# Performance work log

Hardware: AMD Instinct MI355X
Metric: run time of the kernel (lower is better)

Reference implementation:

```python
import jax, jax.numpy as jnp
import numpy as np

B, N, E = 64, 2048, 32768          # graphs, nodes/graph, edges/graph
DIM = 64
RATIO = 0.8
K1 = int(np.ceil(RATIO * N))        # 1639 nodes/graph after pool1
K2 = int(np.ceil(RATIO * K1))       # 1312 nodes/graph after pool2
NUM_CLASSES = 6


def gcn_conv(x, W, b, src, dst, valid, n):
    # GCNConv with self-loops: out = D^-1/2 (A+I) D^-1/2 (x W) + b
    xw = x @ W                                          # [n, DIM]
    deg = jnp.zeros(n, x.dtype).at[dst].add(valid) + 1.0  # in-degree incl. self-loop
    norm = valid * jax.lax.rsqrt(deg[src] * deg[dst])      # per-edge norm (0 for masked)
    agg = jnp.zeros_like(xw).at[dst].add(xw[src] * norm[:, None])
    return agg + xw / deg[:, None] + b                  # self-loop term has norm 1/deg


def topk_pool(x, p, n_graphs, n_per, k):
    # PyG TopKPooling: score = tanh(x.p/||p||); keep top-k per graph; gate x by score
    score = jnp.tanh((x @ p) / jnp.linalg.norm(p))       # [n_graphs*n_per]
    vals, idx = jax.lax.top_k(score.reshape(n_graphs, n_per), k)  # [n_graphs, k]
    xg = x.reshape(n_graphs, n_per, -1)
    sel = jnp.take_along_axis(xg, idx[..., None], axis=1)          # [n_graphs, k, DIM]
    xp = sel * vals[..., None]
    perm = (idx + (jnp.arange(n_graphs) * n_per)[:, None]).reshape(-1)  # global ids kept
    return xp.reshape(n_graphs * k, -1), perm


def global_max_mean(x, n_graphs, n_per):
    xg = x.reshape(n_graphs, n_per, -1)
    return jnp.concatenate([xg.max(axis=1), xg.mean(axis=1)], axis=1)  # [n_graphs, 2*DIM]


def forward(x, edge_index, batch, W1, b1, p1, W2, b2, p2, lin1_w, lin1_b, lin2_w, lin2_b):
    src, dst = edge_index[0], edge_index[1]
    n_total = B * N
    ones = jnp.ones(src.shape[0], x.dtype)

    x = jax.nn.relu(gcn_conv(x, W1, b1, src, dst, ones, n_total))
    x, perm = topk_pool(x, p1, B, N, K1)
    x1 = global_max_mean(x, B, K1)

    # filter_adj: reindex edges to surviving nodes; drop (mask) edges touching removed nodes
    new_id = jnp.full(n_total, -1, jnp.int32).at[perm].set(jnp.arange(B * K1, dtype=jnp.int32))
    s2, d2 = new_id[src], new_id[dst]
    valid = ((s2 >= 0) & (d2 >= 0)).astype(x.dtype)
    s2 = jnp.where(s2 >= 0, s2, 0)
    d2 = jnp.where(d2 >= 0, d2, 0)

    x = jax.nn.relu(gcn_conv(x, W2, b2, s2, d2, valid, B * K1))
    x, _ = topk_pool(x, p2, B, K1, K2)
    x2 = global_max_mean(x, B, K2)

    h = x1 + x2
    h = jax.nn.relu(h @ lin1_w + lin1_b)
    return h @ lin2_w + lin2_b                           # [B, NUM_CLASSES]


def setup_inputs():
    key = jax.random.key(0)
    ks = jax.random.split(key, 10)
    x = jax.random.normal(ks[0], (B * N, DIM), jnp.float32)
    off = (jnp.arange(B) * N)[:, None]
    src = (jax.random.randint(ks[1], (B, E), 0, N) + off).reshape(-1)
    dst = (jax.random.randint(ks[2], (B, E), 0, N) + off).reshape(-1)
    edge_index = jnp.stack([src, dst]).astype(jnp.int32)
    batch = jnp.repeat(jnp.arange(B, dtype=jnp.int32), N)
    s = 1.0 / np.sqrt(DIM)
    return {
        "x": x,
        "edge_index": edge_index,
        "batch": batch,
        "W1": jax.random.normal(ks[3], (DIM, DIM), jnp.float32) * s,
        "b1": jnp.zeros(DIM, jnp.float32),
        "p1": jax.random.normal(ks[4], (DIM,), jnp.float32) * s,
        "W2": jax.random.normal(ks[5], (DIM, DIM), jnp.float32) * s,
        "b2": jnp.zeros(DIM, jnp.float32),
        "p2": jax.random.normal(ks[6], (DIM,), jnp.float32) * s,
        "lin1_w": jax.random.normal(ks[7], (2 * DIM, DIM), jnp.float32) / np.sqrt(2 * DIM),
        "lin1_b": jnp.zeros(DIM, jnp.float32),
        "lin2_w": jax.random.normal(ks[8], (DIM, NUM_CLASSES), jnp.float32) * s,
        "lin2_b": jnp.zeros(NUM_CLASSES, jnp.float32),
    }


def reference(x, edge_index, batch, W1, b1, p1, W2, b2, p2, lin1_w, lin1_b, lin2_w, lin2_b):
    return forward(x, edge_index, batch, W1, b1, p1, W2, b2, p2, lin1_w, lin1_b, lin2_w, lin2_b)
```

## Files before the change

### kernel.cpp

```cpp
#include <hip/hip_runtime.h>
#include <hip/hip_bf16.h>
#include <cstdint>
#include <cstddef>

#define B_    64
#define N_    2048
#define E_    32768
#define DIM_  64
#define K1_   1639
#define K2_   1312
#define NTOT  (B_ * N_)
#define ETOT  (B_ * E_)
#define N2TOT (B_ * K1_)
#define NCLS  6
#define PB_   8
#define CHUNKS_ 16
#define SLICES_ 16
#define BCAP  3072
#define REG_  192

typedef short bf8 __attribute__((ext_vector_type(8)));
typedef float f4  __attribute__((ext_vector_type(4)));

static __device__ __forceinline__ float2 bf2f(unsigned u) {
    float2 r;
    r.x = __uint_as_float(u << 16);
    r.y = __uint_as_float(u & 0xFFFF0000u);
    return r;
}
static __device__ __forceinline__ unsigned f2bf(float a, float b) {
    __hip_bfloat162 h = __float22bfloat162_rn(make_float2(a, b));
    unsigned u;
    __builtin_memcpy(&u, &h, 4);
    return u;
}
static __device__ __forceinline__ unsigned short f2bf_rn(float v) {
    unsigned u = __float_as_uint(v);
    return (unsigned short)((u + 0x7FFFu + ((u >> 16) & 1u)) >> 16);
}

template<int STAGE>
__launch_bounds__(256)
__global__ void k_bucket(const int* src, const int* dst, const int* remap,
                         int* bcnt, unsigned int* blist) {
    const int LSTR = (STAGE == 1) ? 128 : 103;
    __shared__ unsigned int lb[CHUNKS_][REG_];
    __shared__ int lc[CHUNKS_];
    __shared__ int rm[N_];
    int b = blockIdx.x;
    int g = b & 63, slice = b >> 6;
    int tid = threadIdx.x;
    if (tid < CHUNKS_) lc[tid] = 0;
    if (STAGE == 2)
        for (int i = tid; i < N_; i += 256) rm[i] = remap[g * N_ + i];
    __syncthreads();
    const int ESL = E_ / SLICES_;
    const int* sp = src + (size_t)g * E_ + slice * ESL;
    const int* dp = dst + (size_t)g * E_ + slice * ESL;
    int gbase = g * ((STAGE == 1) ? N_ : K1_);
    for (int e = tid * 4; e < ESL; e += 1024) {
        int4 ss = *(const int4*)&sp[e];
        int4 dd = *(const int4*)&dp[e];
#pragma unroll
        for (int t = 0; t < 4; t++) {
            int s = (&ss.x)[t], d = (&dd.x)[t];
            if (STAGE == 2) {
                s = rm[s & (N_ - 1)]; d = rm[d & (N_ - 1)];
                if ((s | d) < 0) continue;
                s -= gbase; d -= gbase;
            } else {
                s &= (N_ - 1); d &= (N_ - 1);
            }
            int ch = d / LSTR;
            int dl = d - ch * LSTR;
            int p = atomicAdd(&lc[ch], 1);
            if (p < REG_) lb[ch][p] = ((unsigned)dl << 12) | (unsigned)s;
        }
    }
    __syncthreads();
    for (int ch = 0; ch < CHUNKS_; ch++) {
        int n = min(lc[ch], REG_);
        unsigned int* out = blist + (size_t)(g * CHUNKS_ + ch) * BCAP + slice * REG_;
        for (int i = tid; i < n; i += 256) out[i] = lb[ch][i];
    }
    if (tid < CHUNKS_) bcnt[(g * SLICES_ + slice) * CHUNKS_ + tid] = min(lc[tid], REG_);
}

template<int STAGE>
__launch_bounds__(256)
__global__ void k_sort(const int* bcnt, unsigned int* blist,
                       const float* xf, const unsigned int* xg,
                       unsigned int* xb, int* ninfo) {
    const int NL   = (STAGE == 1) ? N_ : K1_;
    const int LSTR = (STAGE == 1) ? 128 : 103;
    __shared__ int cnt[128], st[128], cur[128], cnt_s[SLICES_], stot[2];
    __shared__ float rsqv[128];
    __shared__ unsigned short sorted[BCAP];
    int b = blockIdx.x;
    int g = b & 63, ch = b >> 6;
    int tid = threadIdx.x;
    if (tid < 128) { cnt[tid] = 0; cur[tid] = 0; }
    if (tid < SLICES_) cnt_s[tid] = bcnt[(g * SLICES_ + tid) * CHUNKS_ + ch];
    __syncthreads();
    size_t bb = (size_t)(g * CHUNKS_ + ch) * BCAP;
    const unsigned int* bl = blist + bb;
    const int TOT = SLICES_ * REG_;
    for (int i = tid; i < TOT; i += 256) {
        int s = i / REG_, j = i - s * REG_;
        if (j < cnt_s[s]) atomicAdd(&cnt[bl[i] >> 12], 1);
    }
    __syncthreads();
    if (tid < 128) {
        int v = cnt[tid];
        int l64 = tid & 63;
#pragma unroll
        for (int o = 1; o < 64; o <<= 1) {
            int t = __shfl_up(v, o);
            if (l64 >= o) v += t;
        }
        st[tid] = v;
        if (l64 == 63) stot[tid >> 6] = v;
    }
    __syncthreads();
    if (tid >= 64 && tid < 128) st[tid] += stot[0];
    __syncthreads();
    for (int i = tid; i < TOT; i += 256) {
        int s = i / REG_, j = i - s * REG_;
        if (j < cnt_s[s]) {
            unsigned pk = bl[i];
            int dl = (int)(pk >> 12);
            int p = st[dl] - cnt[dl] + atomicAdd(&cur[dl], 1);
            sorted[p] = (unsigned short)(pk & 0xFFFu);
        }
    }
    __syncthreads();
    int n = st[127];
    for (int i = tid; i < n; i += 256) blist[bb + i] = ((unsigned int)sorted[i]) << 5;
    int lo = ch * LSTR;
    int nloc = min(LSTR, NL - lo);
    int gbase = g * NL;
    if (tid < nloc) {
        int node = gbase + lo + tid;
        int c = cnt[tid];
        int start = (int)bb + st[tid] - c;
        ninfo[node] = (start << 8) | min(c, 255);
        rsqv[tid] = rsqrtf((float)(c + 1));
    }
    __syncthreads();
    for (int idx = tid; idx < nloc * 32; idx += 256) {
        int nl = idx >> 5, f2 = idx & 31;
        int node = gbase + lo + nl;
        float sc = rsqv[nl];
        float2 v;
        if (STAGE == 1) v = ((const float2*)xf)[(size_t)node * 32 + f2];
        else            v = bf2f(xg[(size_t)node * 32 + f2]);
        xb[(size_t)node * 32 + f2] = f2bf(v.x * sc, v.y * sc);
    }
}

template<bool GATE>
__launch_bounds__(256)
__global__ void k_agg(const unsigned int* xb, const int* ninfo, const unsigned int* csr,
                      float* y) {
    int b = blockIdx.x;
    int xcd = b & 7, r = b >> 3;
    int graph, local;
    if (GATE) {
        graph = xcd * 8 + r / 410;
        local = (r % 410) * 4 + (threadIdx.x >> 6);
        if (local >= K1_) return;
    } else {
        graph = xcd * 8 + (r >> 9);
        local = (r & 511) * 4 + (threadIdx.x >> 6);
    }
    const int NL = GATE ? K1_ : N_;
    int node = graph * NL + local;
    int lane = threadIdx.x & 63;
    int half = lane >> 5;
    int fpos = lane & 31;
    int ni = ninfo[node];
    int cnt = ni & 255, base = ni >> 8;
    float rd = rsqrtf((float)(cnt + 1));
    float ax = 0.f, ay = 0.f, bx = 0.f, by = 0.f;
    float cx = 0.f, cy = 0.f, dx = 0.f, dy = 0.f;
    int gbase32 = graph * NL * 32;
    for (int chunk = 0; chunk < cnt; chunk += 64) {
        int nch = min(64, cnt - chunk);
        int sv = 0;
        if (lane < nch) sv = gbase32 + (int)csr[base + chunk + lane];
        int i = 0;
        for (; i + 8 <= nch; i += 8) {
            int s0 = __shfl(sv, i + half),     s1 = __shfl(sv, i + 2 + half),
                s2 = __shfl(sv, i + 4 + half), s3 = __shfl(sv, i + 6 + half);
            unsigned u0 = xb[(size_t)(s0 + fpos)];
            unsigned u1 = xb[(size_t)(s1 + fpos)];
            unsigned u2 = xb[(size_t)(s2 + fpos)];
            unsigned u3 = xb[(size_t)(s3 + fpos)];
            float2 f0 = bf2f(u0), f1 = bf2f(u1), f2 = bf2f(u2), f3 = bf2f(u3);
            ax += f0.x; ay += f0.y;
            bx += f1.x; by += f1.y;
            cx += f2.x; cy += f2.y;
            dx += f3.x; dy += f3.y;
        }
        for (; i + 4 <= nch; i += 4) {
            int s0 = __shfl(sv, i + half), s1 = __shfl(sv, i + 2 + half);
            float2 f0 = bf2f(xb[(size_t)(s0 + fpos)]);
            float2 f1 = bf2f(xb[(size_t)(s1 + fpos)]);
            ax += f0.x; ay += f0.y;
            bx += f1.x; by += f1.y;
        }
        for (; i < nch; i += 2) {
            int idx = i + half;
            int s0 = __shfl(sv, idx & 63);
            float m = (idx < nch) ? 1.f : 0.f;
            float2 f0 = bf2f(xb[(size_t)(s0 + fpos)]);
            ax += f0.x * m; ay += f0.y * m;
        }
    }
    float sx = (ax + bx) + (cx + dx), sy = (ay + by) + (cy + dy);
    sx += __shfl(sx, lane ^ 32);
    sy += __shfl(sy, lane ^ 32);
    if (half == 0) {
        float2 fs = bf2f(xb[(size_t)node * 32 + fpos]);
        float2 o;
        o.x = (sx + fs.x) * rd;
        o.y = (sy + fs.y) * rd;
        ((float2*)y)[(size_t)node * 32 + fpos] = o;
    }
}

__launch_bounds__(256)
__global__ void k_convrow(float* y, const float* W, const float* bias, const float* pvec,
                          float* score, int rows) {
    int wid  = threadIdx.x >> 6;
    int lane = threadIdx.x & 63;
    int rowbase = blockIdx.x * 64 + wid * 16;
    int q = lane >> 4, c = lane & 15;
    bf8 bh[2][4], blo[2][4];
#pragma unroll
    for (int ks = 0; ks < 2; ks++)
#pragma unroll
        for (int nt = 0; nt < 4; nt++) {
            bf8 h, l;
#pragma unroll
            for (int j = 0; j < 8; j++) {
                float wv = W[(ks * 32 + q * 8 + j) * 64 + nt * 16 + c];
                unsigned short hb = f2bf_rn(wv);
                h[j] = (short)hb;
                l[j] = (short)f2bf_rn(wv - __uint_as_float((unsigned)hb << 16));
            }
            bh[ks][nt] = h; blo[ks][nt] = l;
        }
    const float* yr = y + (size_t)(rowbase + c) * DIM_ + q * 8;
    bf8 ah[2], al[2];
#pragma unroll
    for (int ks = 0; ks < 2; ks++) {
        float4 v0 = *(const float4*)(yr + ks * 32);
        float4 v1 = *(const float4*)(yr + ks * 32 + 4);
        float vv[8] = {v0.x, v0.y, v0.z, v0.w, v1.x, v1.y, v1.z, v1.w};
        bf8 h, l;
#pragma unroll
        for (int j = 0; j < 8; j++) {
            unsigned short hb = f2bf_rn(vv[j]);
            h[j] = (short)hb;
            l[j] = (short)f2bf_rn(vv[j] - __uint_as_float((unsigned)hb << 16));
        }
        ah[ks] = h; al[ks] = l;
    }
    float pp = 0.f;
#pragma unroll
    for (int i = 0; i < DIM_; i++) pp += pvec[i] * pvec[i];
    float rpn = rsqrtf(pp);
    float dot[4] = {0.f, 0.f, 0.f, 0.f};
#pragma unroll
    for (int nt = 0; nt < 4; nt++) {
        f4 acc = {0.f, 0.f, 0.f, 0.f};
#pragma unroll
        for (int ks = 0; ks < 2; ks++) {
            acc = __builtin_amdgcn_mfma_f32_16x16x32_bf16(ah[ks], bh[ks][nt],  acc, 0, 0, 0);
            acc = __builtin_amdgcn_mfma_f32_16x16x32_bf16(ah[ks], blo[ks][nt], acc, 0, 0, 0);
            acc = __builtin_amdgcn_mfma_f32_16x16x32_bf16(al[ks], bh[ks][nt],  acc, 0, 0, 0);
        }
        float bcol = bias[nt * 16 + c];
        float pcol = pvec[nt * 16 + c];
        float st[4];
#pragma unroll
        for (int reg = 0; reg < 4; reg++) {
            float v = fmaxf(acc[reg] + bcol, 0.f);
            st[reg] = v;
            dot[reg] += v * pcol;
        }
#pragma unroll
        for (int reg = 0; reg < 4; reg++)
            y[(size_t)(rowbase + q * 4 + reg) * DIM_ + nt * 16 + c] = st[reg];
    }
#pragma unroll
    for (int m = 1; m < 16; m <<= 1) {
#pragma unroll
        for (int reg = 0; reg < 4; reg++) dot[reg] += __shfl_xor(dot[reg], m);
    }
    if (c == 0) {
#pragma unroll
        for (int reg = 0; reg < 4; reg++)
            score[rowbase + q * 4 + reg] = tanhf(dot[reg] * rpn);
    }
    (void)rows;
}

template<int STAGE>
__launch_bounds__(256)
__global__ void k_select(const float* score, int* new_id, int* sel, float* vals) {
    const int Nin = (STAGE == 1) ? N_ : K1_;
    const int K   = (STAGE == 1) ? K1_ : K2_;
    __shared__ unsigned long long keys[N_];
    __shared__ int bins[256], wsum[4];
    __shared__ unsigned long long s_prefix;
    __shared__ int s_need, s_cnt;
    int g = blockIdx.x, tid = threadIdx.x;
    int l64 = tid & 63, wid = tid >> 6;
    const float* sg = score + (size_t)g * Nin;
    for (int i = tid; i < Nin; i += 256) {
        unsigned u = __float_as_uint(sg[i]);
        u = (u & 0x80000000u) ? ~u : (u | 0x80000000u);
        keys[i] = ((unsigned long long)u << 11) | (unsigned long long)(2047 - i);
    }
    if (tid == 0) { s_need = K; s_prefix = 0ull; s_cnt = 0; }
    __syncthreads();
    for (int shift = 40; shift >= 0; shift -= 8) {
        bins[tid] = 0;
        __syncthreads();
        unsigned long long pref = s_prefix;
        int need = s_need;
        int hi = shift + 8;
        for (int i = tid; i < Nin; i += 256) {
            unsigned long long k = keys[i];
            if ((k >> hi) == pref) atomicAdd(&bins[(int)((k >> shift) & 255)], 1);
        }
        __syncthreads();
        int mine = bins[tid];
        int v = mine;
#pragma unroll
        for (int o = 1; o < 64; o <<= 1) {
            int t = __shfl_down(v, o);
            if (l64 + o < 64) v += t;
        }
        if (l64 == 0) wsum[wid] = v;
        __syncthreads();
        for (int w = wid + 1; w < 4; w++) v += wsum[w];
        int nxt = v - mine;
        if (v >= need && nxt < need) {
            s_prefix = (pref << 8) | (unsigned long long)tid;
            s_need = need - nxt;
        }
        __syncthreads();
    }
    unsigned long long T = s_prefix;
    for (int i = tid; i < Nin; i += 256) {
        if (keys[i] >= T) {
            int r = atomicAdd(&s_cnt, 1);
            int slot = g * K + r;
            sel[slot]  = g * Nin + i;
            vals[slot] = sg[i];
            if (STAGE == 1) new_id[g * N_ + i] = slot;
        } else if (STAGE == 1) {
            new_id[g * N_ + i] = -1;
        }
    }
}

template<int STAGE>
__launch_bounds__(256)
__global__ void k_pool(const float* conv, const int* sel, const float* vals, float* part,
                       unsigned int* xg) {
    const int K = (STAGE == 1) ? K1_ : K2_;
    int b = blockIdx.x;
    int g = b & 63, c = b >> 6;
    int wv = threadIdx.x >> 6, lane = threadIdx.x & 63;
    float mx = -3.402823466e38f, sm = 0.f;
    for (int r = c * 4 + wv; r < K; r += PB_ * 4) {
        int slot = g * K + r;
        int row  = sel[slot];
        float val = vals[slot];
        float v = conv[(size_t)row * DIM_ + lane] * val;
        mx = fmaxf(mx, v);
        sm += v;
        if (STAGE == 1) {
            unsigned pk = f2bf(v, __shfl_xor(v, 1));
            if (!(lane & 1)) xg[(size_t)slot * 32 + (lane >> 1)] = pk;
        }
    }
    __shared__ float rmx[4][64], rsm[4][64];
    rmx[wv][lane] = mx; rsm[wv][lane] = sm;
    __syncthreads();
    if (wv == 0) {
        mx = fmaxf(fmaxf(rmx[0][lane], rmx[1][lane]), fmaxf(rmx[2][lane], rmx[3][lane]));
        sm = rsm[0][lane] + rsm[1][lane] + rsm[2][lane] + rsm[3][lane];
        part[((size_t)(g * PB_ + c) * 2 + 0) * 64 + lane] = mx;
        part[((size_t)(g * PB_ + c) * 2 + 1) * 64 + lane] = sm;
    }
}

__launch_bounds__(64)
__global__ void k_head(const float* part1, const float* part2,
                       const float* l1w, const float* l1b,
                       const float* l2w, const float* l2b, float* out) {
    __shared__ float h[128];
    __shared__ float h1[64];
    int g = blockIdx.x, t = threadIdx.x;
    float mx1 = -3.402823466e38f, sm1 = 0.f, mx2 = -3.402823466e38f, sm2 = 0.f;
#pragma unroll
    for (int c = 0; c < PB_; c++) {
        mx1 = fmaxf(mx1, part1[((size_t)(g * PB_ + c) * 2 + 0) * 64 + t]);
        sm1 += part1[((size_t)(g * PB_ + c) * 2 + 1) * 64 + t];
        mx2 = fmaxf(mx2, part2[((size_t)(g * PB_ + c) * 2 + 0) * 64 + t]);
        sm2 += part2[((size_t)(g * PB_ + c) * 2 + 1) * 64 + t];
    }
    h[t]      = mx1 + mx2;
    h[t + 64] = sm1 / (float)K1_ + sm2 / (float)K2_;
    __syncthreads();
    float acc = l1b[t];
#pragma unroll 8
    for (int i = 0; i < 128; i++) acc += h[i] * l1w[i * 64 + t];
    h1[t] = fmaxf(acc, 0.0f);
    __syncthreads();
    if (t < NCLS) {
        float o = l2b[t];
#pragma unroll
        for (int i = 0; i < 64; i++) o += h1[i] * l2w[i * NCLS + t];
        out[g * NCLS + t] = o;
    }
}

extern "C" void kernel_launch(void* const* d_in, const int* in_sizes, int n_in,
                              void* d_out, int out_size, void* d_ws, size_t ws_size,
                              hipStream_t stream) {
    const float* x   = (const float*)d_in[0];
    const int*   ei  = (const int*)d_in[1];
    const int*   src = ei;
    const int*   dst = ei + ETOT;
    const float* W1  = (const float*)d_in[3];
    const float* b1  = (const float*)d_in[4];
    const float* p1  = (const float*)d_in[5];
    const float* W2  = (const float*)d_in[6];
    const float* b2  = (const float*)d_in[7];
    const float* p2  = (const float*)d_in[8];
    const float* l1w = (const float*)d_in[9];
    const float* l1b = (const float*)d_in[10];
    const float* l2w = (const float*)d_in[11];
    const float* l2b = (const float*)d_in[12];
    (void)in_sizes; (void)n_in; (void)out_size; (void)ws_size;

    char* ws = (char*)d_ws;
    size_t off = 0;
    auto alloc = [&](size_t bytes) -> void* {
        void* p = ws + off;
        off = (off + bytes + 255) & ~(size_t)255;
        return p;
    };
    float*        bufA  = (float*)       alloc((size_t)NTOT  * DIM_ * 4);
    float*        bufB  = (float*)       alloc((size_t)N2TOT * DIM_ * 4);
    unsigned int* blist = (unsigned int*)alloc((size_t)B_ * CHUNKS_ * BCAP * 4);
    unsigned int* xb    = (unsigned int*)alloc((size_t)NTOT * 32 * 4);
    int*          bcnt  = (int*)         alloc((size_t)B_ * SLICES_ * CHUNKS_ * 4);
    int*          ninfo = (int*)         alloc((size_t)NTOT * 4);
    float*        score = (float*)       alloc((size_t)NTOT * 4);
    int*          newid = (int*)         alloc((size_t)NTOT * 4);
    int*          sel1  = (int*)         alloc((size_t)N2TOT * 4);
    float*        vals1 = (float*)       alloc((size_t)N2TOT * 4);
    int*          sel2  = (int*)         alloc((size_t)B_ * K2_ * 4);
    float*        vals2 = (float*)       alloc((size_t)B_ * K2_ * 4);
    float*        part1 = (float*)       alloc((size_t)B_ * PB_ * 128 * 4);
    float*        part2 = (float*)       alloc((size_t)B_ * PB_ * 128 * 4);
    unsigned int* xg    = (unsigned int*)bufB;

    k_bucket<1><<<B_ * SLICES_, 256, 0, stream>>>(src, dst, nullptr, bcnt, blist);
    k_sort<1><<<B_ * CHUNKS_, 256, 0, stream>>>(bcnt, blist, x, nullptr, xb, ninfo);
    k_agg<false><<<NTOT / 4, 256, 0, stream>>>(xb, ninfo, blist, bufA);
    k_convrow<<<NTOT / 64, 256, 0, stream>>>(bufA, W1, b1, p1, score, NTOT);
    k_select<1><<<B_, 256, 0, stream>>>(score, newid, sel1, vals1);
    k_pool<1><<<B_ * PB_, 256, 0, stream>>>(bufA, sel1, vals1, part1, xg);

    k_bucket<2><<<B_ * SLICES_, 256, 0, stream>>>(src, dst, newid, bcnt, blist);
    k_sort<2><<<B_ * CHUNKS_, 256, 0, stream>>>(bcnt, blist, nullptr, xg, xb, ninfo);
    k_agg<true><<<410 * B_, 256, 0, stream>>>(xb, ninfo, blist, bufB);
    k_convrow<<<N2TOT / 64, 256, 0, stream>>>(bufB, W2, b2, p2, score, N2TOT);
    k_select<2><<<B_, 256, 0, stream>>>(score, nullptr, sel2, vals2);
    k_pool<2><<<B_ * PB_, 256, 0, stream>>>(bufB, sel2, vals2, part2, nullptr);

    k_head<<<B_, 64, 0, stream>>>(part1, part2, l1w, l1b, l2w, l2b, (float*)d_out);
}
```

Before: 344.7 us.

## Fuse sparse aggregation with dense MFMA conv into one per-tile kernel

Merges the gather/aggregate kernel and the row-wise matmul+ReLU+score kernel into a single kernel. Each wave aggregates 16 rows into shared memory, then runs the split-bf16 MFMA transform from there. This removes the fp32 intermediate write and re-read of the aggregated features plus one launch per stage. The aggregation now walks each wave's 16 nodes sequentially, with four edges in flight using 8-byte loads, where before each node had its own wave. That cuts memory-level parallelism per wave and occupancy, and stage 2 needs new tile bounds handling.

Result: slower. 383.8 us (+11.4%).

```diff
diff --git a/kernel.cpp b/kernel.cpp
--- a/kernel.cpp
+++ b/kernel.cpp
@@ -18,6 +18,7 @@
 #define SLICES_ 16
 #define BCAP  3072
 #define REG_  192
+#define T2_   26
 
 typedef short bf8 __attribute__((ext_vector_type(8)));
 typedef float f4  __attribute__((ext_vector_type(4)));
@@ -158,84 +159,84 @@
     }
 }
 
-template<bool GATE>
+template<int STAGE>
 __launch_bounds__(256)
-__global__ void k_agg(const unsigned int* xb, const int* ninfo, const unsigned int* csr,
-                      float* y) {
+__global__ void k_aggconv(const unsigned int* xb, const int* ninfo, const unsigned int* csr,
+                          const float* W, const float* bias, const float* pvec,
+                          float* conv, float* score) {
+    const int NL = (STAGE == 1) ? N_ : K1_;
+    __shared__ float yt[4][16 * 65];
     int b = blockIdx.x;
     int xcd = b & 7, r = b >> 3;
-    int graph, local;
-    if (GATE) {
-        graph = xcd * 8 + r / 410;
-        local = (r % 410) * 4 + (threadIdx.x >> 6);
-        if (local >= K1_) return;
-    } else {
-        graph = xcd * 8 + (r >> 9);
-        local = (r & 511) * 4 + (threadIdx.x >> 6);
-    }
-    const int NL = GATE ? K1_ : N_;
-    int node = graph * NL + local;
-    int lane = threadIdx.x & 63;
-    int half = lane >> 5;
-    int fpos = lane & 31;
-    int ni = ninfo[node];
-    int cnt = ni & 255, base = ni >> 8;
-    float rd = rsqrtf((float)(cnt + 1));
-    float ax = 0.f, ay = 0.f, bx = 0.f, by = 0.f;
-    float cx = 0.f, cy = 0.f, dx = 0.f, dy = 0.f;
-    int gbase32 = graph * NL * 32;
-    for (int chunk = 0; chunk < cnt; chunk += 64) {
-        int nch = min(64, cnt - chunk);
-        int sv = 0;
-        if (lane < nch) sv = gbase32 + (int)csr[base + chunk + lane];
-        int i = 0;
-        for (; i + 8 <= nch; i += 8) {
-            int s0 = __shfl(sv, i + half),     s1 = __shfl(sv, i + 2 + half),
-                s2 = __shfl(sv, i + 4 + half), s3 = __shfl(sv, i + 6 + half);
-            unsigned u0 = xb[(size_t)(s0 + fpos)];
-            unsigned u1 = xb[(size_t)(s1 + fpos)];
-            unsigned u2 = xb[(size_t)(s2 + fpos)];
-            unsigned u3 = xb[(size_t)(s3 + fpos)];
-            float2 f0 = bf2f(u0), f1 = bf2f(u1), f2 = bf2f(u2), f3 = bf2f(u3);
-            ax += f0.x; ay += f0.y;
-            bx += f1.x; by += f1.y;
-            cx += f2.x; cy += f2.y;
-            dx += f3.x; dy += f3.y;
-        }
-        for (; i + 4 <= nch; i += 4) {
-            int s0 = __shfl(sv, i + half), s1 = __shfl(sv, i + 2 + half);
-            float2 f0 = bf2f(xb[(size_t)(s0 + fpos)]);
-            float2 f1 = bf2f(xb[(size_t)(s1 + fpos)]);
-            ax += f0.x; ay += f0.y;
-            bx += f1.x; by += f1.y;
-        }
-        for (; i < nch; i += 2) {
-            int idx = i + half;
-            int s0 = __shfl(sv, idx & 63);
-            float m = (idx < nch) ? 1.f : 0.f;
-            float2 f0 = bf2f(xb[(size_t)(s0 + fpos)]);
-            ax += f0.x * m; ay += f0.y * m;
-        }
-    }
-    float sx = (ax + bx) + (cx + dx), sy = (ay + by) + (cy + dy);
-    sx += __shfl(sx, lane ^ 32);
-    sy += __shfl(sy, lane ^ 32);
-    if (half == 0) {
-        float2 fs = bf2f(xb[(size_t)node * 32 + fpos]);
-        float2 o;
-        o.x = (sx + fs.x) * rd;
-        o.y = (sy + fs.y) * rd;
-        ((float2*)y)[(size_t)node * 32 + fpos] = o;
-    }
-}
-
-__launch_bounds__(256)
-__global__ void k_convrow(float* y, const float* W, const float* bias, const float* pvec,
-                          float* score, int rows) {
+    int graph, tile;
+    if (STAGE == 1) { graph = xcd * 8 + (r >> 5); tile = r & 31; }
+    else            { graph = xcd * 8 + r / T2_;  tile = r % T2_; }
     int wid  = threadIdx.x >> 6;
     int lane = threadIdx.x & 63;
-    int rowbase = blockIdx.x * 64 + wid * 16;
-    int q = lane >> 4, c = lane & 15;
+    int q  = lane >> 4;
+    int fq = lane & 15;
+    int gbase = graph * NL;
+    int gbase32 = gbase * 32;
+    int rowloc0 = tile * 64 + wid * 16;
+
+    for (int j = 0; j < 16; j++) {
+        int local = rowloc0 + j;
+        bool valid = (STAGE == 1) || (local < NL);
+        int node = gbase + (valid ? local : 0);
+        int ni = ninfo[node];
+        int cnt = ni & 255, base = ni >> 8;
+        float rd = valid ? rsqrtf((float)(cnt + 1)) : 0.f;
+        float f0 = 0.f, f1 = 0.f, f2 = 0.f, f3 = 0.f;
+        for (int chunk = 0; chunk < cnt; chunk += 64) {
+            int nch = min(64, cnt - chunk);
+            int sv = 0;
+            if (lane < nch) sv = gbase32 + (int)csr[base + chunk + lane];
+            int i = 0;
+            for (; i + 4 <= nch; i += 4) {
+                int se = __shfl(sv, i + q);
+                uint2 u = *(const uint2*)(xb + se + 2 * fq);
+                float2 aa = bf2f(u.x), bb = bf2f(u.y);
+                f0 += aa.x; f1 += aa.y; f2 += bb.x; f3 += bb.y;
+            }
+            if (i < nch) {
+                int idx = i + q;
+                int se = __shfl(sv, (idx < nch) ? idx : i);
+                float m = (idx < nch) ? 1.f : 0.f;
+                uint2 u = *(const uint2*)(xb + se + 2 * fq);
+                float2 aa = bf2f(u.x), bb = bf2f(u.y);
+                f0 += aa.x * m; f1 += aa.y * m; f2 += bb.x * m; f3 += bb.y * m;
+            }
+        }
+#pragma unroll
+        for (int m = 16; m < 64; m <<= 1) {
+            f0 += __shfl_xor(f0, m);
+            f1 += __shfl_xor(f1, m);
+            f2 += __shfl_xor(f2, m);
+            f3 += __shfl_xor(f3, m);
+        }
+        uint2 us = *(const uint2*)(xb + (size_t)node * 32 + 2 * fq);
+        float2 sa = bf2f(us.x), sb = bf2f(us.y);
+        f0 = (f0 + sa.x) * rd; f1 = (f1 + sa.y) * rd;
+        f2 = (f2 + sb.x) * rd; f3 = (f3 + sb.y) * rd;
+        float wv_ = (q & 1) ? ((q & 2) ? f3 : f1) : ((q & 2) ? f2 : f0);
+        yt[wid][j * 65 + 4 * fq + q] = wv_;
+    }
+    __builtin_amdgcn_sched_barrier(0);
+
+    int c = fq;
+    bf8 ah[2], al[2];
+#pragma unroll
+    for (int ks = 0; ks < 2; ks++) {
+        bf8 h, l;
+#pragma unroll
+        for (int j = 0; j < 8; j++) {
+            float v = yt[wid][c * 65 + ks * 32 + q * 8 + j];
+            unsigned short hb = f2bf_rn(v);
+            h[j] = (short)hb;
+            l[j] = (short)f2bf_rn(v - __uint_as_float((unsigned)hb << 16));
+        }
+        ah[ks] = h; al[ks] = l;
+    }
     bf8 bh[2][4], blo[2][4];
 #pragma unroll
     for (int ks = 0; ks < 2; ks++)
@@ -251,27 +252,12 @@
             }
             bh[ks][nt] = h; blo[ks][nt] = l;
         }
-    const float* yr = y + (size_t)(rowbase + c) * DIM_ + q * 8;
-    bf8 ah[2], al[2];
-#pragma unroll
-    for (int ks = 0; ks < 2; ks++) {
-        float4 v0 = *(const float4*)(yr + ks * 32);
-        float4 v1 = *(const float4*)(yr + ks * 32 + 4);
-        float vv[8] = {v0.x, v0.y, v0.z, v0.w, v1.x, v1.y, v1.z, v1.w};
-        bf8 h, l;
-#pragma unroll
-        for (int j = 0; j < 8; j++) {
-            unsigned short hb = f2bf_rn(vv[j]);
-            h[j] = (short)hb;
-            l[j] = (short)f2bf_rn(vv[j] - __uint_as_float((unsigned)hb << 16));
-        }
-        ah[ks] = h; al[ks] = l;
-    }
     float pp = 0.f;
 #pragma unroll
     for (int i = 0; i < DIM_; i++) pp += pvec[i] * pvec[i];
     float rpn = rsqrtf(pp);
     float dot[4] = {0.f, 0.f, 0.f, 0.f};
+    int growbase = gbase + rowloc0;
 #pragma unroll
     for (int nt = 0; nt < 4; nt++) {
         f4 acc = {0.f, 0.f, 0.f, 0.f};
@@ -283,16 +269,14 @@
         }
         float bcol = bias[nt * 16 + c];
         float pcol = pvec[nt * 16 + c];
-        float st[4];
 #pragma unroll
         for (int reg = 0; reg < 4; reg++) {
             float v = fmaxf(acc[reg] + bcol, 0.f);
-            st[reg] = v;
             dot[reg] += v * pcol;
-        }
-#pragma unroll
-        for (int reg = 0; reg < 4; reg++)
-            y[(size_t)(rowbase + q * 4 + reg) * DIM_ + nt * 16 + c] = st[reg];
+            int rl = rowloc0 + q * 4 + reg;
+            if (STAGE == 1 || rl < NL)
+                conv[(size_t)(gbase + rl) * DIM_ + nt * 16 + c] = v;
+        }
     }
 #pragma unroll
     for (int m = 1; m < 16; m <<= 1) {
@@ -301,10 +285,12 @@
     }
     if (c == 0) {
 #pragma unroll
-        for (int reg = 0; reg < 4; reg++)
-            score[rowbase + q * 4 + reg] = tanhf(dot[reg] * rpn);
-    }
-    (void)rows;
+        for (int reg = 0; reg < 4; reg++) {
+            int rl = rowloc0 + q * 4 + reg;
+            if (STAGE == 1 || rl < NL)
+                score[growbase + q * 4 + reg] = tanhf(dot[reg] * rpn);
+        }
+    }
 }
 
 template<int STAGE>
@@ -475,15 +461,13 @@
 
     k_bucket<1><<<B_ * SLICES_, 256, 0, stream>>>(src, dst, nullptr, bcnt, blist);
     k_sort<1><<<B_ * CHUNKS_, 256, 0, stream>>>(bcnt, blist, x, nullptr, xb, ninfo);
-    k_agg<false><<<NTOT / 4, 256, 0, stream>>>(xb, ninfo, blist, bufA);
-    k_convrow<<<NTOT / 64, 256, 0, stream>>>(bufA, W1, b1, p1, score, NTOT);
+    k_aggconv<1><<<NTOT / 64, 256, 0, stream>>>(xb, ninfo, blist, W1, b1, p1, bufA, score);
     k_select<1><<<B_, 256, 0, stream>>>(score, newid, sel1, vals1);
     k_pool<1><<<B_ * PB_, 256, 0, stream>>>(bufA, sel1, vals1, part1, xg);
 
     k_bucket<2><<<B_ * SLICES_, 256, 0, stream>>>(src, dst, newid, bcnt, blist);
     k_sort<2><<<B_ * CHUNKS_, 256, 0, stream>>>(bcnt, blist, nullptr, xg, xb, ninfo);
-    k_agg<true><<<410 * B_, 256, 0, stream>>>(xb, ninfo, blist, bufB);
-    k_convrow<<<N2TOT / 64, 256, 0, stream>>>(bufB, W2, b2, p2, score, N2TOT);
+    k_aggconv<2><<<B_ * T2_, 256, 0, stream>>>(xb, ninfo, blist, W2, b2, p2, bufB, score);
     k_select<2><<<B_, 256, 0, stream>>>(score, nullptr, sel2, vals2);
     k_pool<2><<<B_ * PB_, 256, 0, stream>>>(bufB, sel2, vals2, part2, nullptr);
 
```

## Fuse top-k select, pooling and MLP head into one per-graph kernel

Applied to the files above, without the earlier changes.

Merges k_select, k_pool and k_head into a single k_selpool kernel per stage. It runs 1024 threads per graph and keeps the selected indices and values in shared memory instead of global sel/vals arrays. This removes three kernel launches and the global round-trips for sel, vals and the partial max/sum buffers, and the head MLP now runs inside the stage-2 kernel. The cost is that pooling parallelism drops from 512 blocks to 64 blocks, so the memory-bound gather over conv rows may underuse the GPU.

Measured after the change: 349.6 us. Within noise of the previous version (+1.4%).

```diff
diff --git a/kernel.cpp b/kernel.cpp
--- a/kernel.cpp
+++ b/kernel.cpp
@@ -13,7 +13,6 @@
 #define ETOT  (B_ * E_)
 #define N2TOT (B_ * K1_)
 #define NCLS  6
-#define PB_   8
 #define CHUNKS_ 16
 #define SLICES_ 16
 #define BCAP  3072
@@ -308,126 +307,124 @@
 }
 
 template<int STAGE>
-__launch_bounds__(256)
-__global__ void k_select(const float* score, int* new_id, int* sel, float* vals) {
+__launch_bounds__(1024)
+__global__ void k_selpool(const float* score, const float* conv, int* new_id,
+                          unsigned int* xg, float* x1,
+                          const float* l1w, const float* l1b,
+                          const float* l2w, const float* l2b, float* out) {
     const int Nin = (STAGE == 1) ? N_ : K1_;
     const int K   = (STAGE == 1) ? K1_ : K2_;
     __shared__ unsigned long long keys[N_];
-    __shared__ int bins[256], wsum[4];
+    __shared__ int bins[256], ts[256], wsum[4];
     __shared__ unsigned long long s_prefix;
     __shared__ int s_need, s_cnt;
+    __shared__ int   lidx[K1_];
+    __shared__ float lval[K1_];
+    __shared__ float rmx[16][64], rsm[16][64];
+    __shared__ float hh[128], h1[64];
     int g = blockIdx.x, tid = threadIdx.x;
-    int l64 = tid & 63, wid = tid >> 6;
+    int wv = tid >> 6, lane = tid & 63;
     const float* sg = score + (size_t)g * Nin;
-    for (int i = tid; i < Nin; i += 256) {
-        unsigned u = __float_as_uint(sg[i]);
-        u = (u & 0x80000000u) ? ~u : (u | 0x80000000u);
-        keys[i] = ((unsigned long long)u << 11) | (unsigned long long)(2047 - i);
+    for (int i = tid; i < N_; i += 1024) {
+        unsigned long long key = 0ull;
+        if (i < Nin) {
+            unsigned u = __float_as_uint(sg[i]);
+            u = (u & 0x80000000u) ? ~u : (u | 0x80000000u);
+            key = ((unsigned long long)u << 11) | (unsigned long long)(2047 - i);
+        }
+        keys[i] = key;
     }
     if (tid == 0) { s_need = K; s_prefix = 0ull; s_cnt = 0; }
+    if (tid < 256) bins[tid] = 0;
     __syncthreads();
     for (int shift = 40; shift >= 0; shift -= 8) {
-        bins[tid] = 0;
-        __syncthreads();
         unsigned long long pref = s_prefix;
         int need = s_need;
         int hi = shift + 8;
-        for (int i = tid; i < Nin; i += 256) {
+        for (int i = tid; i < Nin; i += 1024) {
             unsigned long long k = keys[i];
             if ((k >> hi) == pref) atomicAdd(&bins[(int)((k >> shift) & 255)], 1);
         }
         __syncthreads();
-        int mine = bins[tid];
-        int v = mine;
-#pragma unroll
-        for (int o = 1; o < 64; o <<= 1) {
-            int t = __shfl_down(v, o);
-            if (l64 + o < 64) v += t;
-        }
-        if (l64 == 0) wsum[wid] = v;
-        __syncthreads();
-        for (int w = wid + 1; w < 4; w++) v += wsum[w];
-        int nxt = v - mine;
-        if (v >= need && nxt < need) {
-            s_prefix = (pref << 8) | (unsigned long long)tid;
-            s_need = need - nxt;
-        }
+        if (tid < 256) {
+            int v = bins[tid];
+            int l = tid & 63;
+#pragma unroll
+            for (int o = 1; o < 64; o <<= 1) {
+                int t = __shfl_down(v, o);
+                if (l + o < 64) v += t;
+            }
+            ts[tid] = v;
+            if (l == 0) wsum[tid >> 6] = v;
+        }
+        __syncthreads();
+        if (tid < 256) {
+            int mine = bins[tid];
+            int v = ts[tid];
+            for (int w = (tid >> 6) + 1; w < 4; w++) v += wsum[w];
+            int nxt = v - mine;
+            if (v >= need && nxt < need) {
+                s_prefix = (pref << 8) | (unsigned long long)tid;
+                s_need = need - nxt;
+            }
+        }
+        __syncthreads();
+        if (tid < 256) bins[tid] = 0;
         __syncthreads();
     }
     unsigned long long T = s_prefix;
-    for (int i = tid; i < Nin; i += 256) {
-        if (keys[i] >= T) {
-            int r = atomicAdd(&s_cnt, 1);
-            int slot = g * K + r;
-            sel[slot]  = g * Nin + i;
-            vals[slot] = sg[i];
-            if (STAGE == 1) new_id[g * N_ + i] = slot;
-        } else if (STAGE == 1) {
-            new_id[g * N_ + i] = -1;
-        }
-    }
-}
-
-template<int STAGE>
-__launch_bounds__(256)
-__global__ void k_pool(const float* conv, const int* sel, const float* vals, float* part,
-                       unsigned int* xg) {
-    const int K = (STAGE == 1) ? K1_ : K2_;
-    int b = blockIdx.x;
-    int g = b & 63, c = b >> 6;
-    int wv = threadIdx.x >> 6, lane = threadIdx.x & 63;
+    for (int i = tid; i < Nin; i += 1024) {
+        bool keep = keys[i] >= T;
+        int r = -1;
+        if (keep) {
+            r = atomicAdd(&s_cnt, 1);
+            lidx[r] = i;
+            lval[r] = sg[i];
+        }
+        if (STAGE == 1) new_id[g * N_ + i] = keep ? (g * K1_ + r) : -1;
+    }
+    __syncthreads();
     float mx = -3.402823466e38f, sm = 0.f;
-    for (int r = c * 4 + wv; r < K; r += PB_ * 4) {
-        int slot = g * K + r;
-        int row  = sel[slot];
-        float val = vals[slot];
+    for (int r = wv; r < K; r += 16) {
+        int row = g * Nin + lidx[r];
+        float val = lval[r];
         float v = conv[(size_t)row * DIM_ + lane] * val;
         mx = fmaxf(mx, v);
         sm += v;
         if (STAGE == 1) {
             unsigned pk = f2bf(v, __shfl_xor(v, 1));
-            if (!(lane & 1)) xg[(size_t)slot * 32 + (lane >> 1)] = pk;
-        }
-    }
-    __shared__ float rmx[4][64], rsm[4][64];
+            if (!(lane & 1)) xg[((size_t)(g * K1_ + r)) * 32 + (lane >> 1)] = pk;
+        }
+    }
     rmx[wv][lane] = mx; rsm[wv][lane] = sm;
     __syncthreads();
     if (wv == 0) {
-        mx = fmaxf(fmaxf(rmx[0][lane], rmx[1][lane]), fmaxf(rmx[2][lane], rmx[3][lane]));
-        sm = rsm[0][lane] + rsm[1][lane] + rsm[2][lane] + rsm[3][lane];
-        part[((size_t)(g * PB_ + c) * 2 + 0) * 64 + lane] = mx;
-        part[((size_t)(g * PB_ + c) * 2 + 1) * 64 + lane] = sm;
-    }
-}
-
-__launch_bounds__(64)
-__global__ void k_head(const float* part1, const float* part2,
-                       const float* l1w, const float* l1b,
-                       const float* l2w, const float* l2b, float* out) {
-    __shared__ float h[128];
-    __shared__ float h1[64];
-    int g = blockIdx.x, t = threadIdx.x;
-    float mx1 = -3.402823466e38f, sm1 = 0.f, mx2 = -3.402823466e38f, sm2 = 0.f;
-#pragma unroll
-    for (int c = 0; c < PB_; c++) {
-        mx1 = fmaxf(mx1, part1[((size_t)(g * PB_ + c) * 2 + 0) * 64 + t]);
-        sm1 += part1[((size_t)(g * PB_ + c) * 2 + 1) * 64 + t];
-        mx2 = fmaxf(mx2, part2[((size_t)(g * PB_ + c) * 2 + 0) * 64 + t]);
-        sm2 += part2[((size_t)(g * PB_ + c) * 2 + 1) * 64 + t];
-    }
-    h[t]      = mx1 + mx2;
-    h[t + 64] = sm1 / (float)K1_ + sm2 / (float)K2_;
-    __syncthreads();
-    float acc = l1b[t];
+        mx = rmx[0][lane]; sm = rsm[0][lane];
+#pragma unroll
+        for (int w = 1; w < 16; w++) { mx = fmaxf(mx, rmx[w][lane]); sm += rsm[w][lane]; }
+        if (STAGE == 1) {
+            x1[g * 128 + lane]      = mx;
+            x1[g * 128 + 64 + lane] = sm / (float)K1_;
+        } else {
+            hh[lane]      = x1[g * 128 + lane] + mx;
+            hh[64 + lane] = x1[g * 128 + 64 + lane] + sm / (float)K2_;
+        }
+    }
+    if (STAGE == 2) {
+        __syncthreads();
+        if (wv == 0) {
+            float acc = l1b[lane];
 #pragma unroll 8
-    for (int i = 0; i < 128; i++) acc += h[i] * l1w[i * 64 + t];
-    h1[t] = fmaxf(acc, 0.0f);
-    __syncthreads();
-    if (t < NCLS) {
-        float o = l2b[t];
-#pragma unroll
-        for (int i = 0; i < 64; i++) o += h1[i] * l2w[i * NCLS + t];
-        out[g * NCLS + t] = o;
+            for (int i = 0; i < 128; i++) acc += hh[i] * l1w[i * 64 + lane];
+            h1[lane] = fmaxf(acc, 0.0f);
+        }
+        __syncthreads();
+        if (wv == 0 && lane < NCLS) {
+            float o = l2b[lane];
+#pragma unroll
+            for (int i = 0; i < 64; i++) o += h1[i] * l2w[i * NCLS + lane];
+            out[g * NCLS + lane] = o;
+        }
     }
 }
 
@@ -465,27 +462,20 @@
     int*          ninfo = (int*)         alloc((size_t)NTOT * 4);
     float*        score = (float*)       alloc((size_t)NTOT * 4);
     int*          newid = (int*)         alloc((size_t)NTOT * 4);
-    int*          sel1  = (int*)         alloc((size_t)N2TOT * 4);
-    float*        vals1 = (float*)       alloc((size_t)N2TOT * 4);
-    int*          sel2  = (int*)         alloc((size_t)B_ * K2_ * 4);
-    float*        vals2 = (float*)       alloc((size_t)B_ * K2_ * 4);
-    float*        part1 = (float*)       alloc((size_t)B_ * PB_ * 128 * 4);
-    float*        part2 = (float*)       alloc((size_t)B_ * PB_ * 128 * 4);
+    float*        x1    = (float*)       alloc((size_t)B_ * 128 * 4);
     unsigned int* xg    = (unsigned int*)bufB;
 
     k_bucket<1><<<B_ * SLICES_, 256, 0, stream>>>(src, dst, nullptr, bcnt, blist);
     k_sort<1><<<B_ * CHUNKS_, 256, 0, stream>>>(bcnt, blist, x, nullptr, xb, ninfo);
     k_agg<false><<<NTOT / 4, 256, 0, stream>>>(xb, ninfo, blist, bufA);
     k_convrow<<<NTOT / 64, 256, 0, stream>>>(bufA, W1, b1, p1, score, NTOT);
-    k_select<1><<<B_, 256, 0, stream>>>(score, newid, sel1, vals1);
-    k_pool<1><<<B_ * PB_, 256, 0, stream>>>(bufA, sel1, vals1, part1, xg);
+    k_selpool<1><<<B_, 1024, 0, stream>>>(score, bufA, newid, xg, x1,
+                                          nullptr, nullptr, nullptr, nullptr, nullptr);
 
     k_bucket<2><<<B_ * SLICES_, 256, 0, stream>>>(src, dst, newid, bcnt, blist);
     k_sort<2><<<B_ * CHUNKS_, 256, 0, stream>>>(bcnt, blist, nullptr, xg, xb, ninfo);
     k_agg<true><<<410 * B_, 256, 0, stream>>>(xb, ninfo, blist, bufB);
     k_convrow<<<N2TOT / 64, 256, 0, stream>>>(bufB, W2, b2, p2, score, N2TOT);
-    k_select<2><<<B_, 256, 0, stream>>>(score, nullptr, sel2, vals2);
-    k_pool<2><<<B_ * PB_, 256, 0, stream>>>(bufB, sel2, vals2, part2, nullptr);
-
-    k_head<<<B_, 64, 0, stream>>>(part1, part2, l1w, l1b, l2w, l2b, (float*)d_out);
-}
+    k_selpool<2><<<B_, 1024, 0, stream>>>(score, bufB, nullptr, nullptr, x1,
+                                          l1w, l1b, l2w, l2b, (float*)d_out);
+}
```

## Fuse top-k selection with pooling and use deterministic prefix-sum ranks

Applied to the files above, without the earlier changes.

Merges the per-graph radix top-k select kernel with the pooling kernel. Each of the 8 blocks per graph recomputes the threshold redundantly and then pools only its own contiguous node range, reading scores and rows directly. Stage 1 replaces atomic slot assignment with a block prefix scan, so kept nodes stay in index order. This removes two launches and the sel/vals round trips through global memory, and it raises select parallelism from 64 to 512 blocks. The cost is 8x redundant radix-select work per graph and extra shared memory for the rank array.

After: 335.9 us. 2.5% less time.

```diff
diff --git a/kernel.cpp b/kernel.cpp
--- a/kernel.cpp
+++ b/kernel.cpp
@@ -309,22 +309,32 @@
 
 template<int STAGE>
 __launch_bounds__(256)
-__global__ void k_select(const float* score, int* new_id, int* sel, float* vals) {
+__global__ void k_selpool(const float* score, const float* conv, int* new_id,
+                          unsigned int* xg, float* part) {
     const int Nin = (STAGE == 1) ? N_ : K1_;
     const int K   = (STAGE == 1) ? K1_ : K2_;
+    const int RNG = (STAGE == 1) ? (N_ / PB_) : ((K1_ + PB_ - 1) / PB_);
     __shared__ unsigned long long keys[N_];
     __shared__ int bins[256], wsum[4];
     __shared__ unsigned long long s_prefix;
-    __shared__ int s_need, s_cnt;
-    int g = blockIdx.x, tid = threadIdx.x;
+    __shared__ int s_need;
+    __shared__ int rnk[N_];
+    __shared__ float rmx[4][64], rsm[4][64];
+    int b = blockIdx.x;
+    int g = b & 63, pb = b >> 6;
+    int tid = threadIdx.x;
     int l64 = tid & 63, wid = tid >> 6;
     const float* sg = score + (size_t)g * Nin;
-    for (int i = tid; i < Nin; i += 256) {
-        unsigned u = __float_as_uint(sg[i]);
-        u = (u & 0x80000000u) ? ~u : (u | 0x80000000u);
-        keys[i] = ((unsigned long long)u << 11) | (unsigned long long)(2047 - i);
-    }
-    if (tid == 0) { s_need = K; s_prefix = 0ull; s_cnt = 0; }
+    for (int i = tid; i < N_; i += 256) {
+        unsigned long long key = 0ull;
+        if (i < Nin) {
+            unsigned u = __float_as_uint(sg[i]);
+            u = (u & 0x80000000u) ? ~u : (u | 0x80000000u);
+            key = ((unsigned long long)u << 11) | (unsigned long long)(2047 - i);
+        }
+        keys[i] = key;
+    }
+    if (tid == 0) { s_need = K; s_prefix = 0ull; }
     __syncthreads();
     for (int shift = 40; shift >= 0; shift -= 8) {
         bins[tid] = 0;
@@ -355,48 +365,51 @@
         __syncthreads();
     }
     unsigned long long T = s_prefix;
-    for (int i = tid; i < Nin; i += 256) {
-        if (keys[i] >= T) {
-            int r = atomicAdd(&s_cnt, 1);
-            int slot = g * K + r;
-            sel[slot]  = g * Nin + i;
-            vals[slot] = sg[i];
-            if (STAGE == 1) new_id[g * N_ + i] = slot;
-        } else if (STAGE == 1) {
-            new_id[g * N_ + i] = -1;
-        }
-    }
-}
-
-template<int STAGE>
-__launch_bounds__(256)
-__global__ void k_pool(const float* conv, const int* sel, const float* vals, float* part,
-                       unsigned int* xg) {
-    const int K = (STAGE == 1) ? K1_ : K2_;
-    int b = blockIdx.x;
-    int g = b & 63, c = b >> 6;
-    int wv = threadIdx.x >> 6, lane = threadIdx.x & 63;
+    if (STAGE == 1) {
+        int base8 = tid * 8;
+        int loc[8];
+        int c8 = 0;
+#pragma unroll
+        for (int j = 0; j < 8; j++) { loc[j] = c8; c8 += (keys[base8 + j] >= T) ? 1 : 0; }
+        int v = c8;
+#pragma unroll
+        for (int o = 1; o < 64; o <<= 1) {
+            int t = __shfl_up(v, o);
+            if (l64 >= o) v += t;
+        }
+        if (l64 == 63) wsum[wid] = v;
+        __syncthreads();
+        int wbase = 0;
+        for (int w = 0; w < wid; w++) wbase += wsum[w];
+        int exc = wbase + v - c8;
+#pragma unroll
+        for (int j = 0; j < 8; j++) rnk[base8 + j] = exc + loc[j];
+        __syncthreads();
+        int i = pb * RNG + tid;
+        bool keep = keys[i] >= T;
+        new_id[g * N_ + i] = keep ? (g * K1_ + rnk[i]) : -1;
+    }
+    int R0 = pb * RNG;
+    int R1 = min(R0 + RNG, Nin);
     float mx = -3.402823466e38f, sm = 0.f;
-    for (int r = c * 4 + wv; r < K; r += PB_ * 4) {
-        int slot = g * K + r;
-        int row  = sel[slot];
-        float val = vals[slot];
-        float v = conv[(size_t)row * DIM_ + lane] * val;
+    for (int i = R0 + wid; i < R1; i += 4) {
+        if (keys[i] < T) continue;
+        float val = sg[i];
+        float v = conv[(size_t)(g * Nin + i) * DIM_ + l64] * val;
         mx = fmaxf(mx, v);
         sm += v;
         if (STAGE == 1) {
             unsigned pk = f2bf(v, __shfl_xor(v, 1));
-            if (!(lane & 1)) xg[(size_t)slot * 32 + (lane >> 1)] = pk;
-        }
-    }
-    __shared__ float rmx[4][64], rsm[4][64];
-    rmx[wv][lane] = mx; rsm[wv][lane] = sm;
-    __syncthreads();
-    if (wv == 0) {
-        mx = fmaxf(fmaxf(rmx[0][lane], rmx[1][lane]), fmaxf(rmx[2][lane], rmx[3][lane]));
-        sm = rsm[0][lane] + rsm[1][lane] + rsm[2][lane] + rsm[3][lane];
-        part[((size_t)(g * PB_ + c) * 2 + 0) * 64 + lane] = mx;
-        part[((size_t)(g * PB_ + c) * 2 + 1) * 64 + lane] = sm;
+            if (!(l64 & 1)) xg[(size_t)(g * K1_ + rnk[i]) * 32 + (l64 >> 1)] = pk;
+        }
+    }
+    rmx[wid][l64] = mx; rsm[wid][l64] = sm;
+    __syncthreads();
+    if (wid == 0) {
+        mx = fmaxf(fmaxf(rmx[0][l64], rmx[1][l64]), fmaxf(rmx[2][l64], rmx[3][l64]));
+        sm = rsm[0][l64] + rsm[1][l64] + rsm[2][l64] + rsm[3][l64];
+        part[((size_t)(g * PB_ + pb) * 2 + 0) * 64 + l64] = mx;
+        part[((size_t)(g * PB_ + pb) * 2 + 1) * 64 + l64] = sm;
     }
 }
 
@@ -465,10 +478,6 @@
     int*          ninfo = (int*)         alloc((size_t)NTOT * 4);
     float*        score = (float*)       alloc((size_t)NTOT * 4);
     int*          newid = (int*)         alloc((size_t)NTOT * 4);
-    int*          sel1  = (int*)         alloc((size_t)N2TOT * 4);
-    float*        vals1 = (float*)       alloc((size_t)N2TOT * 4);
-    int*          sel2  = (int*)         alloc((size_t)B_ * K2_ * 4);
-    float*        vals2 = (float*)       alloc((size_t)B_ * K2_ * 4);
     float*        part1 = (float*)       alloc((size_t)B_ * PB_ * 128 * 4);
     float*        part2 = (float*)       alloc((size_t)B_ * PB_ * 128 * 4);
     unsigned int* xg    = (unsigned int*)bufB;
@@ -477,15 +486,13 @@
     k_sort<1><<<B_ * CHUNKS_, 256, 0, stream>>>(bcnt, blist, x, nullptr, xb, ninfo);
     k_agg<false><<<NTOT / 4, 256, 0, stream>>>(xb, ninfo, blist, bufA);
     k_convrow<<<NTOT / 64, 256, 0, stream>>>(bufA, W1, b1, p1, score, NTOT);
-    k_select<1><<<B_, 256, 0, stream>>>(score, newid, sel1, vals1);
-    k_pool<1><<<B_ * PB_, 256, 0, stream>>>(bufA, sel1, vals1, part1, xg);
+    k_selpool<1><<<B_ * PB_, 256, 0, stream>>>(score, bufA, newid, xg, part1);
 
     k_bucket<2><<<B_ * SLICES_, 256, 0, stream>>>(src, dst, newid, bcnt, blist);
     k_sort<2><<<B_ * CHUNKS_, 256, 0, stream>>>(bcnt, blist, nullptr, xg, xb, ninfo);
     k_agg<true><<<410 * B_, 256, 0, stream>>>(xb, ninfo, blist, bufB);
     k_convrow<<<N2TOT / 64, 256, 0, stream>>>(bufB, W2, b2, p2, score, N2TOT);
-    k_select<2><<<B_, 256, 0, stream>>>(score, nullptr, sel2, vals2);
-    k_pool<2><<<B_ * PB_, 256, 0, stream>>>(bufB, sel2, vals2, part2, nullptr);
+    k_selpool<2><<<B_ * PB_, 256, 0, stream>>>(score, bufB, nullptr, nullptr, part2);
 
     k_head<<<B_, 64, 0, stream>>>(part1, part2, l1w, l1b, l2w, l2b, (float*)d_out);
 }
```
